# Kernel tuning notes

Hardware: AMD Instinct MI355X
Metric: run time of the kernel (lower is better)

Reference implementation:

```python
import jax, jax.numpy as jnp
import numpy as np

# NOTE: ffn(in, out, capacity=1, activation) is assumed to be a single Linear(in, out)
# followed by the activation (ReLU). Dropout is identity in eval mode.

B, M, H, Eh = 16, 128, 256, 128

def setup_inputs() -> dict:
    key = jax.random.key(0)
    ks = jax.random.split(key, 12)
    s = lambda n: 1.0 / np.sqrt(n)
    return {
        "X": jax.random.normal(ks[0], (B, M, H), jnp.float32),
        "E": jax.random.normal(ks[1], (B, M, M, Eh), jnp.float32),
        "A": jax.random.uniform(ks[2], (B, M, M), jnp.float32),
        "eps": jnp.zeros((1,), jnp.float32),
        "We": jax.random.normal(ks[3], (Eh, Eh), jnp.float32) * s(Eh),
        "be": jnp.zeros((Eh,), jnp.float32),
        "Wr": jax.random.normal(ks[4], (H + Eh, H), jnp.float32) * s(H + Eh),
        "br": jnp.zeros((H,), jnp.float32),
        "W0": jax.random.normal(ks[5], (H, H), jnp.float32) * s(H),
        "b0": jnp.zeros((H,), jnp.float32),
        "W1": jax.random.normal(ks[6], (H, H), jnp.float32) * s(H),
        "b1": jnp.zeros((H,), jnp.float32),
    }

def reference(X, E, A, eps, We, be, Wr, br, W0, b0, W1, b1):
    act = jax.nn.relu
    # edge_mapper: ffn(e, e, capacity=1) -> Linear + activation
    Em = act(jnp.einsum('bije,ef->bijf', E, We) + be)          # (b,m,m,e)
    # msg[b,j,:] = sum_i A[b,i,j] * cat(X[b,i,:], Em[b,i,j,:])
    # fused: avoids materializing the (b,m,m,h+e) intermediate
    msg_x = jnp.einsum('bij,bih->bjh', A, X)                   # (b,m,h)
    msg_e = jnp.einsum('bij,bije->bje', A, Em)                 # (b,m,e)
    msg = jnp.concatenate([msg_x, msg_e], axis=-1)             # (b,m,h+e)
    Xs = (1.0 + eps) * X
    out = Xs + act(jnp.einsum('bmc,ch->bmh', msg, Wr) + br)    # residual_mapping
    out = jnp.einsum('bmh,hk->bmk', out, W0) + b0
    out = act(out)  # dropout p is identity in eval mode
    out = jnp.einsum('bmh,hk->bmk', out, W1) + b1
    out = act(out)
    return out
```

## Files before the change

kernel.cpp:

```cpp
#include <hip/hip_runtime.h>

typedef float        f32x4  __attribute__((ext_vector_type(4)));
typedef __bf16       bf16x8 __attribute__((ext_vector_type(8)));
typedef unsigned int u32x2  __attribute__((ext_vector_type(2)));
typedef unsigned int u32x4  __attribute__((ext_vector_type(4)));
typedef unsigned short u16;

#define MFMA16(a,b,c) __builtin_amdgcn_mfma_f32_16x16x32_bf16((a),(b),(c),0,0,0)

__device__ __forceinline__ unsigned bf_rnd(float x) {
    unsigned u = __float_as_uint(x);
    return (u + 0x7FFFu + ((u >> 16) & 1u)) & 0xFFFF0000u;
}
__device__ __forceinline__ void split_bf(float x, unsigned &h, unsigned &l) {
    unsigned hr = bf_rnd(x);
    h = hr >> 16;
    float lo = x - __uint_as_float(hr);
    l = bf_rnd(lo) >> 16;
}
__device__ __forceinline__ void split4(const f32x4 v, u32x2 &hp, u32x2 &lp) {
    unsigned h0,l0,h1,l1,h2,l2,h3,l3;
    split_bf(v[0],h0,l0); split_bf(v[1],h1,l1);
    split_bf(v[2],h2,l2); split_bf(v[3],h3,l3);
    hp[0] = h0 | (h1 << 16); hp[1] = h2 | (h3 << 16);
    lp[0] = l0 | (l1 << 16); lp[1] = l2 | (l3 << 16);
}

__device__ __forceinline__ bf16x8 ldfrag(const u16* base, int row, int kb) {
    int off = ((row << 8) + kb) ^ ((row & 7) << 4);
    return __builtin_bit_cast(bf16x8, *(const u32x4*)((const char*)base + off));
}
__device__ __forceinline__ void stlds8(u16* base, int row, int colbyte, u32x2 v) {
    int off = ((row << 8) + colbyte) ^ ((row & 7) << 4);
    *(u32x2*)((char*)base + off) = v;
}

__global__ __launch_bounds__(256, 1) void k_edge(
    const float* __restrict__ E, const float* __restrict__ A,
    const float* __restrict__ We, const float* __restrict__ be,
    float* __restrict__ part)
{
    __shared__ __align__(16) u16 sEhi[128*128];
    __shared__ __align__(16) u16 sElo[128*128];
    __shared__ __align__(16) u16 sWhi[128*128];
    __shared__ __align__(16) u16 sWlo[128*128];
    __shared__ __align__(16) float sA[128];
    __shared__ float sBe[128];

    const int tid  = threadIdx.x;
    const int lane = tid & 63;
    const int wid  = tid >> 6;
    const int wm   = (wid >> 1) << 6;
    const int wn   = (wid & 1)  << 6;
    const int b    = blockIdx.x >> 4;
    const int c    = blockIdx.x & 15;
    const int i0   = c << 3;

    {
        const int f  = tid & 127;
        const int eo = tid >> 7;
        #pragma unroll
        for (int q = 0; q < 16; ++q) {
            const int eq = eo + q*2;
            const int e0 = eq << 2;
            f32x4 w;
            w[0] = We[(e0+0)*128 + f];
            w[1] = We[(e0+1)*128 + f];
            w[2] = We[(e0+2)*128 + f];
            w[3] = We[(e0+3)*128 + f];
            u32x2 hp, lp; split4(w, hp, lp);
            stlds8(sWhi, f, e0*2, hp);
            stlds8(sWlo, f, e0*2, lp);
        }
        if (tid < 128) sBe[tid] = be[tid];
    }

    const float* Eb = E + (size_t)(b*128 + i0) * 16384;
    f32x4 ebuf[16];
    #pragma unroll
    for (int s = 0; s < 16; ++s)
        ebuf[s] = *(const f32x4*)(Eb + (size_t)(tid + s*256)*4);
    f32x4 abuf = {};
    if (tid < 32) abuf = *(const f32x4*)(A + (size_t)(b*128 + i0)*128 + tid*4);

    __syncthreads();

    float be_r[4];
    #pragma unroll
    for (int n = 0; n < 4; ++n) be_r[n] = sBe[wn + n*16 + (lane & 15)];

    f32x4 P[4][4] = {};

    for (int it = 0; it < 8; ++it) {
        #pragma unroll
        for (int s = 0; s < 16; ++s) {
            const int flat4 = tid + s*256;
            const int row = flat4 >> 5;
            const int cb  = (flat4 & 31) << 3;
            u32x2 hp, lp; split4(ebuf[s], hp, lp);
            stlds8(sEhi, row, cb, hp);
            stlds8(sElo, row, cb, lp);
        }
        if (tid < 32) *(f32x4*)(sA + tid*4) = abuf;
        if (it < 7) {
            const float* En = Eb + (size_t)(it+1)*16384;
            #pragma unroll
            for (int s = 0; s < 16; ++s)
                ebuf[s] = *(const f32x4*)(En + (size_t)(tid + s*256)*4);
            if (tid < 32)
                abuf = *(const f32x4*)(A + (size_t)(b*128 + i0 + it + 1)*128 + tid*4);
        }
        __syncthreads();

        f32x4 em[4][4] = {};
        #pragma unroll
        for (int k = 0; k < 4; ++k) {
            const int kb = (k << 6) + ((lane >> 4) << 4);
            bf16x8 eh[4], el[4], wh[4], wl[4];
            #pragma unroll
            for (int m = 0; m < 4; ++m) {
                const int row = wm + m*16 + (lane & 15);
                eh[m] = ldfrag(sEhi, row, kb);
                el[m] = ldfrag(sElo, row, kb);
            }
            #pragma unroll
            for (int n = 0; n < 4; ++n) {
                const int row = wn + n*16 + (lane & 15);
                wh[n] = ldfrag(sWhi, row, kb);
                wl[n] = ldfrag(sWlo, row, kb);
            }
            #pragma unroll
            for (int m = 0; m < 4; ++m)
                #pragma unroll
                for (int n = 0; n < 4; ++n) {
                    em[m][n] = MFMA16(eh[m], wh[n], em[m][n]);
                    em[m][n] = MFMA16(eh[m], wl[n], em[m][n]);
                    em[m][n] = MFMA16(el[m], wh[n], em[m][n]);
                }
        }
        #pragma unroll
        for (int m = 0; m < 4; ++m) {
            const f32x4 a4 = *(const f32x4*)(sA + wm + m*16 + ((lane >> 4) << 2));
            #pragma unroll
            for (int n = 0; n < 4; ++n)
                #pragma unroll
                for (int r = 0; r < 4; ++r) {
                    float v = em[m][n][r] + be_r[n];
                    v = fmaxf(v, 0.0f);
                    P[m][n][r] += a4[r] * v;
                }
        }
        __syncthreads();
    }

    float* op = part + (size_t)blockIdx.x * 16384;
    #pragma unroll
    for (int m = 0; m < 4; ++m) {
        const int jb = wm + m*16 + ((lane >> 4) << 2);
        #pragma unroll
        for (int r = 0; r < 4; ++r)
            #pragma unroll
            for (int n = 0; n < 4; ++n)
                op[(jb + r)*128 + wn + n*16 + (lane & 15)] = P[m][n][r];
    }
}

__global__ __launch_bounds__(256) void k_msg(
    const float* __restrict__ A, const float* __restrict__ X,
    const float* __restrict__ part, float* __restrict__ msg)
{
    __shared__ float sAt[128*16];
    const int tid = threadIdx.x;
    const int b   = blockIdx.x >> 3;
    const int jt  = blockIdx.x & 7;
    const int j0  = jt << 4;

    #pragma unroll
    for (int p = 0; p < 8; ++p) {
        const int j = j0 + (tid >> 7) + p*2;
        const int f = tid & 127;
        float s = 0.f;
        #pragma unroll
        for (int cc = 0; cc < 16; ++cc)
            s += part[(size_t)((b*16 + cc)*128 + j)*128 + f];
        msg[(size_t)(b*128 + j)*384 + 256 + f] = s;
    }

    #pragma unroll
    for (int s = 0; s < 8; ++s) {
        const int i = s*16 + (tid >> 4);
        sAt[i*16 + (tid & 15)] = A[(size_t)(b*128 + i)*128 + j0 + (tid & 15)];
    }
    __syncthreads();

    const int h = tid;
    float acc[16];
    #pragma unroll
    for (int jj = 0; jj < 16; ++jj) acc[jj] = 0.f;
    for (int i = 0; i < 128; ++i) {
        const float x = X[(size_t)(b*128 + i)*256 + h];
        #pragma unroll
        for (int jj = 0; jj < 16; ++jj)
            acc[jj] += sAt[i*16 + jj] * x;
    }
    #pragma unroll
    for (int jj = 0; jj < 16; ++jj)
        msg[(size_t)(b*128 + j0 + jj)*384 + h] = acc[jj];
}

template<int KT, bool RES>
__global__ __launch_bounds__(256) void k_tail(
    const float* __restrict__ In, const float* __restrict__ W,
    const float* __restrict__ bias, const float* __restrict__ res,
    const float* __restrict__ epsp, float* __restrict__ out)
{
    __shared__ __align__(16) u16 sAhi[64*128], sAlo[64*128];
    __shared__ __align__(16) u16 sBhi[64*128], sBlo[64*128];
    const int tid  = threadIdx.x;
    const int lane = tid & 63;
    const int wid  = tid >> 6;
    const int wm   = (wid >> 1) << 5;
    const int wn   = (wid & 1)  << 5;
    const int r0   = blockIdx.x << 6;
    const int h0   = blockIdx.y << 6;

    f32x4 P[2][2] = {};

    for (int k0 = 0; k0 < KT; k0 += 128) {
        #pragma unroll
        for (int s = 0; s < 8; ++s) {
            const int row = (tid >> 5) + s*8;
            const int q   = tid & 31;
            f32x4 v = *(const f32x4*)(In + (size_t)(r0 + row)*KT + k0 + q*4);
            u32x2 hp, lp; split4(v, hp, lp);
            stlds8(sAhi, row, q << 3, hp);
            stlds8(sAlo, row, q << 3, lp);
        }
        #pragma unroll
        for (int s = 0; s < 8; ++s) {
            const int n  = tid & 63;
            const int kq = (tid >> 6) + s*4;
            const int kk = k0 + kq*4;
            f32x4 w;
            w[0] = W[(size_t)(kk+0)*256 + h0 + n];
            w[1] = W[(size_t)(kk+1)*256 + h0 + n];
            w[2] = W[(size_t)(kk+2)*256 + h0 + n];
            w[3] = W[(size_t)(kk+3)*256 + h0 + n];
            u32x2 hp, lp; split4(w, hp, lp);
            stlds8(sBhi, n, kq << 3, hp);
            stlds8(sBlo, n, kq << 3, lp);
        }
        __syncthreads();

        #pragma unroll
        for (int k = 0; k < 4; ++k) {
            const int kb = (k << 6) + ((lane >> 4) << 4);
            bf16x8 ah[2], al[2], bh[2], bl[2];
            #pragma unroll
            for (int m = 0; m < 2; ++m) {
                const int row = wm + m*16 + (lane & 15);
                ah[m] = ldfrag(sAhi, row, kb);
                al[m] = ldfrag(sAlo, row, kb);
            }
            #pragma unroll
            for (int n = 0; n < 2; ++n) {
                const int row = wn + n*16 + (lane & 15);
                bh[n] = ldfrag(sBhi, row, kb);
                bl[n] = ldfrag(sBlo, row, kb);
            }
            #pragma unroll
            for (int m = 0; m < 2; ++m)
                #pragma unroll
                for (int n = 0; n < 2; ++n) {
                    P[m][n] = MFMA16(ah[m], bh[n], P[m][n]);
                    P[m][n] = MFMA16(ah[m], bl[n], P[m][n]);
                    P[m][n] = MFMA16(al[m], bh[n], P[m][n]);
                }
        }
        __syncthreads();
    }

    const float eps = RES ? epsp[0] : 0.f;
    #pragma unroll
    for (int m = 0; m < 2; ++m)
        #pragma unroll
        for (int n = 0; n < 2; ++n) {
            const int hcol = h0 + wn + n*16 + (lane & 15);
            const float bv = bias[hcol];
            #pragma unroll
            for (int e = 0; e < 4; ++e) {
                const int r = r0 + wm + m*16 + ((lane >> 4) << 2) + e;
                float v = fmaxf(P[m][n][e] + bv, 0.f);
                if (RES) v += (1.f + eps) * res[(size_t)r*256 + hcol];
                out[(size_t)r*256 + hcol] = v;
            }
        }
}

extern "C" void kernel_launch(void* const* d_in, const int* in_sizes, int n_in,
                              void* d_out, int out_size, void* d_ws, size_t ws_size,
                              hipStream_t stream)
{
    const float* X   = (const float*)d_in[0];
    const float* E   = (const float*)d_in[1];
    const float* A   = (const float*)d_in[2];
    const float* eps = (const float*)d_in[3];
    const float* We  = (const float*)d_in[4];
    const float* be  = (const float*)d_in[5];
    const float* Wr  = (const float*)d_in[6];
    const float* br  = (const float*)d_in[7];
    const float* W0  = (const float*)d_in[8];
    const float* b0  = (const float*)d_in[9];
    const float* W1  = (const float*)d_in[10];
    const float* b1  = (const float*)d_in[11];
    float* out = (float*)d_out;

    float* part = (float*)d_ws;
    float* msg  = part + 16*16*128*128;
    float* out1 = msg  + 2048*384;
    float* out2 = out1 + 2048*256;

    k_edge<<<256, 256, 0, stream>>>(E, A, We, be, part);
    k_msg <<<128, 256, 0, stream>>>(A, X, part, msg);
    k_tail<384, true ><<<dim3(32,4), 256, 0, stream>>>(msg,  Wr, br, X, eps, out1);
    k_tail<256, false><<<dim3(32,4), 256, 0, stream>>>(out1, W0, b0, nullptr, nullptr, out2);
    k_tail<256, false><<<dim3(32,4), 256, 0, stream>>>(out2, W1, b1, nullptr, nullptr, out);
}
```

Baseline: 271.7 us.

## Pre-split weights to bf16 hi/lo and load MFMA fragments directly from global

Adds a prep kernel that transposes all weights and splits them into bf16 hi/lo once per call. The edge kernel drops LDS staging and loads E fragments straight into registers in MFMA layout, with 512 threads per block. The message and MLP stages now write hi/lo bf16 intermediates, so the tail GEMMs read fragments from global with no LDS and run on smaller tiles over more blocks. This removes the LDS round trips and repeated per-tile splitting, at the cost of an extra launch and uncoalesced row-strided global fragment loads.

```diff
diff --git a/kernel.cpp b/kernel.cpp
--- a/kernel.cpp
+++ b/kernel.cpp
@@ -2,7 +2,6 @@
 
 typedef float        f32x4  __attribute__((ext_vector_type(4)));
 typedef __bf16       bf16x8 __attribute__((ext_vector_type(8)));
-typedef unsigned int u32x2  __attribute__((ext_vector_type(2)));
 typedef unsigned int u32x4  __attribute__((ext_vector_type(4)));
 typedef unsigned short u16;
 
@@ -18,283 +17,255 @@
     float lo = x - __uint_as_float(hr);
     l = bf_rnd(lo) >> 16;
 }
-__device__ __forceinline__ void split4(const f32x4 v, u32x2 &hp, u32x2 &lp) {
-    unsigned h0,l0,h1,l1,h2,l2,h3,l3;
-    split_bf(v[0],h0,l0); split_bf(v[1],h1,l1);
-    split_bf(v[2],h2,l2); split_bf(v[3],h3,l3);
-    hp[0] = h0 | (h1 << 16); hp[1] = h2 | (h3 << 16);
-    lp[0] = l0 | (l1 << 16); lp[1] = l2 | (l3 << 16);
-}
-
-__device__ __forceinline__ bf16x8 ldfrag(const u16* base, int row, int kb) {
-    int off = ((row << 8) + kb) ^ ((row & 7) << 4);
-    return __builtin_bit_cast(bf16x8, *(const u32x4*)((const char*)base + off));
-}
-__device__ __forceinline__ void stlds8(u16* base, int row, int colbyte, u32x2 v) {
-    int off = ((row << 8) + colbyte) ^ ((row & 7) << 4);
-    *(u32x2*)((char*)base + off) = v;
-}
-
-__global__ __launch_bounds__(256, 1) void k_edge(
+__device__ __forceinline__ void split8(const f32x4 a, const f32x4 b, bf16x8 &hv, bf16x8 &lv) {
+    u32x4 hp, lp;
+    unsigned h0,l0,h1,l1;
+    split_bf(a[0],h0,l0); split_bf(a[1],h1,l1); hp[0]=h0|(h1<<16); lp[0]=l0|(l1<<16);
+    split_bf(a[2],h0,l0); split_bf(a[3],h1,l1); hp[1]=h0|(h1<<16); lp[1]=l0|(l1<<16);
+    split_bf(b[0],h0,l0); split_bf(b[1],h1,l1); hp[2]=h0|(h1<<16); lp[2]=l0|(l1<<16);
+    split_bf(b[2],h0,l0); split_bf(b[3],h1,l1); hp[3]=h0|(h1<<16); lp[3]=l0|(l1<<16);
+    hv = __builtin_bit_cast(bf16x8, hp);
+    lv = __builtin_bit_cast(bf16x8, lp);
+}
+__device__ __forceinline__ bf16x8 ld16(const u16* p) {
+    return __builtin_bit_cast(bf16x8, *(const u32x4*)p);
+}
+
+__global__ __launch_bounds__(256) void k_prep(
+    const float* __restrict__ We, const float* __restrict__ Wr,
+    const float* __restrict__ W0, const float* __restrict__ W1,
+    u16* __restrict__ WeTh, u16* __restrict__ WeTl,
+    u16* __restrict__ WrTh, u16* __restrict__ WrTl,
+    u16* __restrict__ W0Th, u16* __restrict__ W0Tl,
+    u16* __restrict__ W1Th, u16* __restrict__ W1Tl)
+{
+    int t = blockIdx.x * 256 + threadIdx.x;
+    float v; u16 *dh, *dl; int dst;
+    if (t < 16384) {
+        int f = t & 127, e = t >> 7;
+        v = We[e*128 + f]; dst = f*128 + e; dh = WeTh; dl = WeTl;
+    } else if (t < 16384 + 98304) {
+        int u = t - 16384; int h = u & 255, k = u >> 8;
+        v = Wr[k*256 + h]; dst = h*384 + k; dh = WrTh; dl = WrTl;
+    } else if (t < 16384 + 98304 + 65536) {
+        int u = t - 16384 - 98304; int h = u & 255, k = u >> 8;
+        v = W0[k*256 + h]; dst = h*256 + k; dh = W0Th; dl = W0Tl;
+    } else {
+        int u = t - 16384 - 98304 - 65536; int h = u & 255, k = u >> 8;
+        v = W1[k*256 + h]; dst = h*256 + k; dh = W1Th; dl = W1Tl;
+    }
+    unsigned hh, ll; split_bf(v, hh, ll);
+    dh[dst] = (u16)hh; dl[dst] = (u16)ll;
+}
+
+__global__ __launch_bounds__(512, 2) void k_edge(
     const float* __restrict__ E, const float* __restrict__ A,
-    const float* __restrict__ We, const float* __restrict__ be,
-    float* __restrict__ part)
-{
-    __shared__ __align__(16) u16 sEhi[128*128];
-    __shared__ __align__(16) u16 sElo[128*128];
-    __shared__ __align__(16) u16 sWhi[128*128];
-    __shared__ __align__(16) u16 sWlo[128*128];
-    __shared__ __align__(16) float sA[128];
-    __shared__ float sBe[128];
-
-    const int tid  = threadIdx.x;
-    const int lane = tid & 63;
-    const int wid  = tid >> 6;
-    const int wm   = (wid >> 1) << 6;
-    const int wn   = (wid & 1)  << 6;
-    const int b    = blockIdx.x >> 4;
-    const int c    = blockIdx.x & 15;
-    const int i0   = c << 3;
-
-    {
-        const int f  = tid & 127;
-        const int eo = tid >> 7;
-        #pragma unroll
-        for (int q = 0; q < 16; ++q) {
-            const int eq = eo + q*2;
-            const int e0 = eq << 2;
-            f32x4 w;
-            w[0] = We[(e0+0)*128 + f];
-            w[1] = We[(e0+1)*128 + f];
-            w[2] = We[(e0+2)*128 + f];
-            w[3] = We[(e0+3)*128 + f];
-            u32x2 hp, lp; split4(w, hp, lp);
-            stlds8(sWhi, f, e0*2, hp);
-            stlds8(sWlo, f, e0*2, lp);
-        }
-        if (tid < 128) sBe[tid] = be[tid];
-    }
-
-    const float* Eb = E + (size_t)(b*128 + i0) * 16384;
-    f32x4 ebuf[16];
-    #pragma unroll
-    for (int s = 0; s < 16; ++s)
-        ebuf[s] = *(const f32x4*)(Eb + (size_t)(tid + s*256)*4);
-    f32x4 abuf = {};
-    if (tid < 32) abuf = *(const f32x4*)(A + (size_t)(b*128 + i0)*128 + tid*4);
-
-    __syncthreads();
-
-    float be_r[4];
-    #pragma unroll
-    for (int n = 0; n < 4; ++n) be_r[n] = sBe[wn + n*16 + (lane & 15)];
-
-    f32x4 P[4][4] = {};
-
-    for (int it = 0; it < 8; ++it) {
-        #pragma unroll
-        for (int s = 0; s < 16; ++s) {
-            const int flat4 = tid + s*256;
-            const int row = flat4 >> 5;
-            const int cb  = (flat4 & 31) << 3;
-            u32x2 hp, lp; split4(ebuf[s], hp, lp);
-            stlds8(sEhi, row, cb, hp);
-            stlds8(sElo, row, cb, lp);
-        }
-        if (tid < 32) *(f32x4*)(sA + tid*4) = abuf;
-        if (it < 7) {
-            const float* En = Eb + (size_t)(it+1)*16384;
-            #pragma unroll
-            for (int s = 0; s < 16; ++s)
-                ebuf[s] = *(const f32x4*)(En + (size_t)(tid + s*256)*4);
-            if (tid < 32)
-                abuf = *(const f32x4*)(A + (size_t)(b*128 + i0 + it + 1)*128 + tid*4);
-        }
-        __syncthreads();
-
-        f32x4 em[4][4] = {};
-        #pragma unroll
-        for (int k = 0; k < 4; ++k) {
-            const int kb = (k << 6) + ((lane >> 4) << 4);
-            bf16x8 eh[4], el[4], wh[4], wl[4];
-            #pragma unroll
-            for (int m = 0; m < 4; ++m) {
-                const int row = wm + m*16 + (lane & 15);
-                eh[m] = ldfrag(sEhi, row, kb);
-                el[m] = ldfrag(sElo, row, kb);
-            }
-            #pragma unroll
-            for (int n = 0; n < 4; ++n) {
-                const int row = wn + n*16 + (lane & 15);
-                wh[n] = ldfrag(sWhi, row, kb);
-                wl[n] = ldfrag(sWlo, row, kb);
-            }
-            #pragma unroll
-            for (int m = 0; m < 4; ++m)
-                #pragma unroll
-                for (int n = 0; n < 4; ++n) {
-                    em[m][n] = MFMA16(eh[m], wh[n], em[m][n]);
-                    em[m][n] = MFMA16(eh[m], wl[n], em[m][n]);
-                    em[m][n] = MFMA16(el[m], wh[n], em[m][n]);
-                }
-        }
-        #pragma unroll
-        for (int m = 0; m < 4; ++m) {
-            const f32x4 a4 = *(const f32x4*)(sA + wm + m*16 + ((lane >> 4) << 2));
-            #pragma unroll
-            for (int n = 0; n < 4; ++n)
-                #pragma unroll
-                for (int r = 0; r < 4; ++r) {
-                    float v = em[m][n][r] + be_r[n];
-                    v = fmaxf(v, 0.0f);
-                    P[m][n][r] += a4[r] * v;
-                }
-        }
-        __syncthreads();
-    }
-
-    float* op = part + (size_t)blockIdx.x * 16384;
-    #pragma unroll
-    for (int m = 0; m < 4; ++m) {
-        const int jb = wm + m*16 + ((lane >> 4) << 2);
-        #pragma unroll
-        for (int r = 0; r < 4; ++r)
-            #pragma unroll
-            for (int n = 0; n < 4; ++n)
-                op[(jb + r)*128 + wn + n*16 + (lane & 15)] = P[m][n][r];
-    }
-}
-
-__global__ __launch_bounds__(256) void k_msg(
-    const float* __restrict__ A, const float* __restrict__ X,
-    const float* __restrict__ part, float* __restrict__ msg)
-{
-    __shared__ float sAt[128*16];
-    const int tid = threadIdx.x;
-    const int b   = blockIdx.x >> 3;
-    const int jt  = blockIdx.x & 7;
-    const int j0  = jt << 4;
-
-    #pragma unroll
-    for (int p = 0; p < 8; ++p) {
-        const int j = j0 + (tid >> 7) + p*2;
-        const int f = tid & 127;
-        float s = 0.f;
-        #pragma unroll
-        for (int cc = 0; cc < 16; ++cc)
-            s += part[(size_t)((b*16 + cc)*128 + j)*128 + f];
-        msg[(size_t)(b*128 + j)*384 + 256 + f] = s;
-    }
-
-    #pragma unroll
-    for (int s = 0; s < 8; ++s) {
-        const int i = s*16 + (tid >> 4);
-        sAt[i*16 + (tid & 15)] = A[(size_t)(b*128 + i)*128 + j0 + (tid & 15)];
-    }
-    __syncthreads();
-
-    const int h = tid;
-    float acc[16];
-    #pragma unroll
-    for (int jj = 0; jj < 16; ++jj) acc[jj] = 0.f;
-    for (int i = 0; i < 128; ++i) {
-        const float x = X[(size_t)(b*128 + i)*256 + h];
-        #pragma unroll
-        for (int jj = 0; jj < 16; ++jj)
-            acc[jj] += sAt[i*16 + jj] * x;
-    }
-    #pragma unroll
-    for (int jj = 0; jj < 16; ++jj)
-        msg[(size_t)(b*128 + j0 + jj)*384 + h] = acc[jj];
-}
-
-template<int KT, bool RES>
-__global__ __launch_bounds__(256) void k_tail(
-    const float* __restrict__ In, const float* __restrict__ W,
-    const float* __restrict__ bias, const float* __restrict__ res,
-    const float* __restrict__ epsp, float* __restrict__ out)
-{
-    __shared__ __align__(16) u16 sAhi[64*128], sAlo[64*128];
-    __shared__ __align__(16) u16 sBhi[64*128], sBlo[64*128];
+    const u16* __restrict__ WeTh, const u16* __restrict__ WeTl,
+    const float* __restrict__ be, float* __restrict__ part)
+{
     const int tid  = threadIdx.x;
     const int lane = tid & 63;
     const int wid  = tid >> 6;
     const int wm   = (wid >> 1) << 5;
-    const int wn   = (wid & 1)  << 5;
-    const int r0   = blockIdx.x << 6;
-    const int h0   = blockIdx.y << 6;
-
-    f32x4 P[2][2] = {};
-
-    for (int k0 = 0; k0 < KT; k0 += 128) {
-        #pragma unroll
-        for (int s = 0; s < 8; ++s) {
-            const int row = (tid >> 5) + s*8;
-            const int q   = tid & 31;
-            f32x4 v = *(const f32x4*)(In + (size_t)(r0 + row)*KT + k0 + q*4);
-            u32x2 hp, lp; split4(v, hp, lp);
-            stlds8(sAhi, row, q << 3, hp);
-            stlds8(sAlo, row, q << 3, lp);
-        }
-        #pragma unroll
-        for (int s = 0; s < 8; ++s) {
-            const int n  = tid & 63;
-            const int kq = (tid >> 6) + s*4;
-            const int kk = k0 + kq*4;
-            f32x4 w;
-            w[0] = W[(size_t)(kk+0)*256 + h0 + n];
-            w[1] = W[(size_t)(kk+1)*256 + h0 + n];
-            w[2] = W[(size_t)(kk+2)*256 + h0 + n];
-            w[3] = W[(size_t)(kk+3)*256 + h0 + n];
-            u32x2 hp, lp; split4(w, hp, lp);
-            stlds8(sBhi, n, kq << 3, hp);
-            stlds8(sBlo, n, kq << 3, lp);
-        }
-        __syncthreads();
-
-        #pragma unroll
-        for (int k = 0; k < 4; ++k) {
-            const int kb = (k << 6) + ((lane >> 4) << 4);
-            bf16x8 ah[2], al[2], bh[2], bl[2];
-            #pragma unroll
-            for (int m = 0; m < 2; ++m) {
-                const int row = wm + m*16 + (lane & 15);
-                ah[m] = ldfrag(sAhi, row, kb);
-                al[m] = ldfrag(sAlo, row, kb);
+    const int wn   = (wid & 1)  << 6;
+    const int lrow = lane & 15;
+    const int lk   = lane >> 4;
+    const int b    = blockIdx.x >> 4;
+    const int c    = blockIdx.x & 15;
+    const int i0   = c << 3;
+
+    float ber[4];
+    #pragma unroll
+    for (int n = 0; n < 4; ++n) ber[n] = be[wn + n*16 + lrow];
+
+    const float* Eb = E + (size_t)(b*128 + i0) * 16384;
+
+    f32x4 eb[16];
+    {
+        const float* Es = Eb;
+        #pragma unroll
+        for (int m = 0; m < 2; ++m)
+            #pragma unroll
+            for (int k = 0; k < 4; ++k) {
+                const float* p = Es + (wm + m*16 + lrow)*128 + k*32 + lk*8;
+                eb[(m*4+k)*2+0] = *(const f32x4*)p;
+                eb[(m*4+k)*2+1] = *(const f32x4*)(p+4);
             }
-            #pragma unroll
-            for (int n = 0; n < 2; ++n) {
-                const int row = wn + n*16 + (lane & 15);
-                bh[n] = ldfrag(sBhi, row, kb);
-                bl[n] = ldfrag(sBlo, row, kb);
-            }
+    }
+
+    f32x4 P[2][4] = {};
+
+    for (int s = 0; s < 8; ++s) {
+        bf16x8 ehf[8], elf[8];
+        #pragma unroll
+        for (int q = 0; q < 8; ++q)
+            split8(eb[q*2+0], eb[q*2+1], ehf[q], elf[q]);
+
+        if (s < 7) {
+            const float* Es = Eb + (size_t)(s+1)*16384;
             #pragma unroll
             for (int m = 0; m < 2; ++m)
                 #pragma unroll
-                for (int n = 0; n < 2; ++n) {
-                    P[m][n] = MFMA16(ah[m], bh[n], P[m][n]);
-                    P[m][n] = MFMA16(ah[m], bl[n], P[m][n]);
-                    P[m][n] = MFMA16(al[m], bh[n], P[m][n]);
+                for (int k = 0; k < 4; ++k) {
+                    const float* p = Es + (wm + m*16 + lrow)*128 + k*32 + lk*8;
+                    eb[(m*4+k)*2+0] = *(const f32x4*)p;
+                    eb[(m*4+k)*2+1] = *(const f32x4*)(p+4);
                 }
         }
+
+        f32x4 em[2][4] = {};
+        #pragma unroll
+        for (int k = 0; k < 4; ++k) {
+            bf16x8 wh[4], wl[4];
+            #pragma unroll
+            for (int n = 0; n < 4; ++n) {
+                const int off = (wn + n*16 + lrow)*128 + k*32 + lk*8;
+                wh[n] = ld16(WeTh + off);
+                wl[n] = ld16(WeTl + off);
+            }
+            #pragma unroll
+            for (int m = 0; m < 2; ++m)
+                #pragma unroll
+                for (int n = 0; n < 4; ++n) {
+                    em[m][n] = MFMA16(ehf[m*4+k], wh[n], em[m][n]);
+                    em[m][n] = MFMA16(ehf[m*4+k], wl[n], em[m][n]);
+                    em[m][n] = MFMA16(elf[m*4+k], wh[n], em[m][n]);
+                }
+        }
+
+        const int i = i0 + s;
+        #pragma unroll
+        for (int m = 0; m < 2; ++m) {
+            const f32x4 a4 = *(const f32x4*)(A + (size_t)(b*128 + i)*128 + wm + m*16 + lk*4);
+            #pragma unroll
+            for (int n = 0; n < 4; ++n)
+                #pragma unroll
+                for (int r = 0; r < 4; ++r) {
+                    float v = fmaxf(em[m][n][r] + ber[n], 0.0f);
+                    P[m][n][r] += a4[r] * v;
+                }
+        }
+    }
+
+    float* op = part + (size_t)blockIdx.x * 16384;
+    #pragma unroll
+    for (int m = 0; m < 2; ++m)
+        #pragma unroll
+        for (int r = 0; r < 4; ++r) {
+            const int j = wm + m*16 + lk*4 + r;
+            #pragma unroll
+            for (int n = 0; n < 4; ++n)
+                op[j*128 + wn + n*16 + lrow] = P[m][n][r];
+        }
+}
+
+__global__ __launch_bounds__(256) void k_msg(
+    const float* __restrict__ A, const float* __restrict__ X,
+    const float* __restrict__ part,
+    u16* __restrict__ msg_h, u16* __restrict__ msg_l)
+{
+    const int bid = blockIdx.x;
+    const int tid = threadIdx.x;
+    __shared__ float sAt[128*8];
+
+    if (bid < 1024) {
+        const int b = bid >> 6, jp = bid & 63;
+        const int j = jp*2 + (tid >> 7), f = tid & 127;
+        const float* p = part + (size_t)b*16*16384 + j*128 + f;
+        float s = 0.f;
+        #pragma unroll
+        for (int cc = 0; cc < 16; ++cc) s += p[(size_t)cc*16384];
+        unsigned hh, ll; split_bf(s, hh, ll);
+        const size_t o = (size_t)(b*128 + j)*384 + 256 + f;
+        msg_h[o] = (u16)hh; msg_l[o] = (u16)ll;
+    } else {
+        const int idx = bid - 1024;
+        const int b = idx >> 4, jt = idx & 15, j0 = jt << 3;
+        #pragma unroll
+        for (int q = 0; q < 4; ++q) {
+            const int e = tid + q*256;
+            sAt[e] = A[(size_t)(b*128 + (e >> 3))*128 + j0 + (e & 7)];
+        }
         __syncthreads();
+        const int h = tid;
+        float acc[8] = {};
+        const float* Xb = X + (size_t)b*128*256 + h;
+        #pragma unroll 4
+        for (int i = 0; i < 128; ++i) {
+            const float x = Xb[(size_t)i*256];
+            #pragma unroll
+            for (int jj = 0; jj < 8; ++jj) acc[jj] += sAt[i*8 + jj] * x;
+        }
+        #pragma unroll
+        for (int jj = 0; jj < 8; ++jj) {
+            unsigned hh, ll; split_bf(acc[jj], hh, ll);
+            const size_t o = (size_t)(b*128 + j0 + jj)*384 + h;
+            msg_h[o] = (u16)hh; msg_l[o] = (u16)ll;
+        }
+    }
+}
+
+template<int KT, bool RES, bool F32OUT>
+__global__ __launch_bounds__(256) void k_tail(
+    const u16* __restrict__ Ah, const u16* __restrict__ Al,
+    const u16* __restrict__ Bh, const u16* __restrict__ Bl,
+    const float* __restrict__ bias, const float* __restrict__ res,
+    const float* __restrict__ epsp,
+    float* __restrict__ outf, u16* __restrict__ oh, u16* __restrict__ ol)
+{
+    const int tid  = threadIdx.x;
+    const int lane = tid & 63;
+    const int wid  = tid >> 6;
+    const int lrow = lane & 15;
+    const int lk   = lane >> 4;
+    const int wm   = (wid >> 1) << 4;
+    const int wn   = (wid & 1)  << 5;
+    const int r0   = blockIdx.x << 5;
+    const int h0   = blockIdx.y << 6;
+
+    const int arow = r0 + wm + lrow;
+    const u16* pah = Ah + (size_t)arow*KT + lk*8;
+    const u16* pal = Al + (size_t)arow*KT + lk*8;
+    const int c0 = h0 + wn + lrow;
+    const u16* pb0h = Bh + (size_t)c0*KT + lk*8;
+    const u16* pb0l = Bl + (size_t)c0*KT + lk*8;
+    const u16* pb1h = pb0h + 16*KT;
+    const u16* pb1l = pb0l + 16*KT;
+
+    f32x4 P[2] = {};
+    #pragma unroll
+    for (int ks = 0; ks < KT/32; ++ks) {
+        const bf16x8 ah = ld16(pah + ks*32);
+        const bf16x8 al = ld16(pal + ks*32);
+        const bf16x8 b0h = ld16(pb0h + ks*32), b0l = ld16(pb0l + ks*32);
+        const bf16x8 b1h = ld16(pb1h + ks*32), b1l = ld16(pb1l + ks*32);
+        P[0] = MFMA16(ah, b0h, P[0]);
+        P[0] = MFMA16(ah, b0l, P[0]);
+        P[0] = MFMA16(al, b0h, P[0]);
+        P[1] = MFMA16(ah, b1h, P[1]);
+        P[1] = MFMA16(ah, b1l, P[1]);
+        P[1] = MFMA16(al, b1h, P[1]);
     }
 
     const float eps = RES ? epsp[0] : 0.f;
     #pragma unroll
-    for (int m = 0; m < 2; ++m)
-        #pragma unroll
-        for (int n = 0; n < 2; ++n) {
-            const int hcol = h0 + wn + n*16 + (lane & 15);
-            const float bv = bias[hcol];
-            #pragma unroll
-            for (int e = 0; e < 4; ++e) {
-                const int r = r0 + wm + m*16 + ((lane >> 4) << 2) + e;
-                float v = fmaxf(P[m][n][e] + bv, 0.f);
-                if (RES) v += (1.f + eps) * res[(size_t)r*256 + hcol];
-                out[(size_t)r*256 + hcol] = v;
+    for (int n = 0; n < 2; ++n) {
+        const int col = h0 + wn + n*16 + lrow;
+        const float bv = bias[col];
+        #pragma unroll
+        for (int e = 0; e < 4; ++e) {
+            const int r = r0 + wm + lk*4 + e;
+            float v = fmaxf(P[n][e] + bv, 0.f);
+            if (RES) v += (1.f + eps) * res[(size_t)r*256 + col];
+            if (F32OUT) {
+                outf[(size_t)r*256 + col] = v;
+            } else {
+                unsigned hh, ll; split_bf(v, hh, ll);
+                oh[(size_t)r*256 + col] = (u16)hh;
+                ol[(size_t)r*256 + col] = (u16)ll;
             }
         }
+    }
 }
 
 extern "C" void kernel_launch(void* const* d_in, const int* in_sizes, int n_in,
@@ -315,14 +286,24 @@
     const float* b1  = (const float*)d_in[11];
     float* out = (float*)d_out;
 
-    float* part = (float*)d_ws;
-    float* msg  = part + 16*16*128*128;
-    float* out1 = msg  + 2048*384;
-    float* out2 = out1 + 2048*256;
-
-    k_edge<<<256, 256, 0, stream>>>(E, A, We, be, part);
-    k_msg <<<128, 256, 0, stream>>>(A, X, part, msg);
-    k_tail<384, true ><<<dim3(32,4), 256, 0, stream>>>(msg,  Wr, br, X, eps, out1);
-    k_tail<256, false><<<dim3(32,4), 256, 0, stream>>>(out1, W0, b0, nullptr, nullptr, out2);
-    k_tail<256, false><<<dim3(32,4), 256, 0, stream>>>(out2, W1, b1, nullptr, nullptr, out);
-}
+    u16* w = (u16*)d_ws;
+    u16* WeTh = w;              u16* WeTl = WeTh + 16384;
+    u16* WrTh = WeTl + 16384;   u16* WrTl = WrTh + 98304;
+    u16* W0Th = WrTl + 98304;   u16* W0Tl = W0Th + 65536;
+    u16* W1Th = W0Tl + 65536;   u16* W1Tl = W1Th + 65536;
+    u16* msg_h = W1Tl + 65536;  u16* msg_l = msg_h + 786432;
+    u16* o1h = msg_l + 786432;  u16* o1l = o1h + 524288;
+    u16* o2h = o1l + 524288;    u16* o2l = o2h + 524288;
+    float* part = (float*)(o2l + 524288);
+
+    k_prep<<<960, 256, 0, stream>>>(We, Wr, W0, W1,
+        WeTh, WeTl, WrTh, WrTl, W0Th, W0Tl, W1Th, W1Tl);
+    k_edge<<<256, 512, 0, stream>>>(E, A, WeTh, WeTl, be, part);
+    k_msg<<<1280, 256, 0, stream>>>(A, X, part, msg_h, msg_l);
+    k_tail<384, true , false><<<dim3(64,4), 256, 0, stream>>>(
+        msg_h, msg_l, WrTh, WrTl, br, X, eps, nullptr, o1h, o1l);
+    k_tail<256, false, false><<<dim3(64,4), 256, 0, stream>>>(
+        o1h, o1l, W0Th, W0Tl, b0, nullptr, nullptr, nullptr, o2h, o2l);
+    k_tail<256, false, true ><<<dim3(64,4), 256, 0, stream>>>(
+        o2h, o2l, W1Th, W1Tl, b1, nullptr, nullptr, out, nullptr, nullptr);
+}
```

Measured after the change: 399.7 us. 1.47x slower.
